# Optimization experiments

Hardware: AMD Instinct MI355X
Metric: run time of the kernel (lower is better)

Reference implementation:

```python
import jax, jax.numpy as jnp
import numpy as np

N = 20000      # nodes
E = 640000     # edges
F = 128        # input features
H = 256        # hidden dim
G = 64         # graphs in batch


def setup_inputs() -> dict:
    key = jax.random.key(0)
    ks = jax.random.split(key, 24)
    w = lambda k, sh: (jax.random.normal(k, sh, jnp.float32) * 0.05)
    inp = {
        'x': jax.random.normal(ks[0], (N, F), jnp.float32),
        'edge_index': jax.random.randint(ks[1], (2, E), 0, N, dtype=jnp.int32),
        'batch': jnp.sort(jax.random.randint(ks[2], (N,), 0, G, dtype=jnp.int32)),
        # GCN stack
        'gcn_w1': w(ks[3], (F, H)), 'gcn_b1': jnp.zeros((H,), jnp.float32),
        'gcn_w2': w(ks[4], (H, H)), 'gcn_b2': jnp.zeros((H,), jnp.float32),
        'gcn_w3': w(ks[5], (H, H)), 'gcn_b3': jnp.zeros((H,), jnp.float32),
        'gcn_w4': w(ks[6], (H, H)), 'gcn_b4': jnp.zeros((H,), jnp.float32),
        # EdgeConv 1: Linear(2F,H) -> ReLU -> Linear(H,H)
        'ec1_w1': w(ks[7], (2 * F, H)), 'ec1_b1': jnp.zeros((H,), jnp.float32),
        'ec1_w2': w(ks[8], (H, H)),     'ec1_b2': jnp.zeros((H,), jnp.float32),
        # EdgeConv 2: Linear(2H,H) -> ReLU -> Linear(H,H)
        'ec2_w1': w(ks[9], (2 * H, H)), 'ec2_b1': jnp.zeros((H,), jnp.float32),
        'ec2_w2': w(ks[10], (H, H)),    'ec2_b2': jnp.zeros((H,), jnp.float32),
        # head
        'fc1_w': w(ks[11], (2 * H, H)), 'fc1_b': jnp.zeros((H,), jnp.float32),
        'out_w': w(ks[12], (H, 1)),     'out_b': jnp.zeros((1,), jnp.float32),
    }
    return inp


def _gcn_conv(x, W, b, src, dst, n):
    # PyG GCNConv: add self loops, symmetric deg^-1/2 normalization, scatter-sum.
    h = x @ W                                        # [n, H]
    loops = jnp.arange(n, dtype=src.dtype)
    s = jnp.concatenate([src, loops])
    d = jnp.concatenate([dst, loops])
    deg = jax.ops.segment_sum(jnp.ones(s.shape[0], x.dtype), d, num_segments=n)
    dinv = jnp.where(deg > 0, jax.lax.rsqrt(deg), 0.0)
    norm = (dinv[s] * dinv[d])[:, None]              # [E+n, 1]
    return jax.ops.segment_sum(h[s] * norm, d, num_segments=n) + b


def _edge_conv(x, w1, b1, w2, b2, src, dst, n):
    # PyG EdgeConv: msg = MLP([x_i, x_j - x_i]), max-aggregate at target i.
    xi = x[dst]
    xj = x[src]
    m = jnp.concatenate([xi, xj - xi], axis=1)       # [E, 2*d]
    m = jax.nn.relu(m @ w1 + b1) @ w2 + b2           # [E, H]
    out = jax.ops.segment_max(m, dst, num_segments=n)
    return jnp.where(jnp.isfinite(out), out, 0.0)    # empty segments -> 0


def reference(x, edge_index, batch,
              gcn_w1, gcn_b1, gcn_w2, gcn_b2, gcn_w3, gcn_b3, gcn_w4, gcn_b4,
              ec1_w1, ec1_b1, ec1_w2, ec1_b2, ec2_w1, ec2_b1, ec2_w2, ec2_b2,
              fc1_w, fc1_b, out_w, out_b):
    n = x.shape[0]
    src, dst = edge_index[0], edge_index[1]
    relu = jax.nn.relu
    # GCN branch (dropout is identity at inference)
    xg = relu(_gcn_conv(x, gcn_w1, gcn_b1, src, dst, n))
    xg = relu(_gcn_conv(xg, gcn_w2, gcn_b2, src, dst, n))
    xg = relu(_gcn_conv(xg, gcn_w3, gcn_b3, src, dst, n))
    xg = relu(_gcn_conv(xg, gcn_w4, gcn_b4, src, dst, n))
    # EdgeConv branch
    xe = relu(_edge_conv(x, ec1_w1, ec1_b1, ec1_w2, ec1_b2, src, dst, n))
    xe = relu(_edge_conv(xe, ec2_w1, ec2_b1, ec2_w2, ec2_b2, src, dst, n))
    # pool per graph + head
    x_cat = jnp.concatenate([xg, xe], axis=1)        # [n, 512]
    g = jax.ops.segment_sum(x_cat, batch, num_segments=G)  # [G, 512]
    g = relu(g @ fc1_w + fc1_b)
    return g @ out_w + out_b                          # [G, 1]
```

## Files before the change

### kernel.cpp

```cpp
#include <hip/hip_runtime.h>

#define HD 256

typedef __attribute__((ext_vector_type(8))) __bf16 bf16x8;
typedef __attribute__((ext_vector_type(4))) float f32x4;

static __device__ __forceinline__ float relu_f(float x){ return x > 0.f ? x : 0.f; }

static __device__ __forceinline__ void split_cvt(const float* m8, bf16x8& vh, bf16x8& vl){
    #pragma unroll
    for (int j = 0; j < 8; j++){
        float m = m8[j];
        __bf16 h = (__bf16)m;
        vh[j] = h;
        vl[j] = (__bf16)(m - (float)h);
    }
}

__global__ void k_count(const int* __restrict__ dst, int* __restrict__ cnt, int E){
    int i = blockIdx.x * blockDim.x + threadIdx.x;
    if (i < E) atomicAdd(&cnt[dst[i]], 1);
}

__global__ void k_dinv(const int* __restrict__ cnt, float* __restrict__ dinv, int n){
    int i = blockIdx.x * blockDim.x + threadIdx.x;
    if (i < n) dinv[i] = 1.0f / sqrtf((float)(cnt[i] + 1));
}

__global__ void k_scan(const int* __restrict__ cnt, int* __restrict__ row_ptr, int n){
    __shared__ int lds[1024];
    int t = threadIdx.x;
    int carry = 0;
    for (int base = 0; base < n; base += 1024){
        int idx = base + t;
        int v = (idx < n) ? cnt[idx] : 0;
        __syncthreads();
        lds[t] = v;
        __syncthreads();
        for (int off = 1; off < 1024; off <<= 1){
            int add = (t >= off) ? lds[t - off] : 0;
            __syncthreads();
            lds[t] += add;
            __syncthreads();
        }
        int incl = lds[t];
        if (idx < n) row_ptr[idx] = carry + incl - v;
        carry += lds[1023];
    }
    if (t == 0) row_ptr[n] = carry;
}

__global__ void k_fill(const int* __restrict__ src, const int* __restrict__ dst,
                       const int* __restrict__ row_ptr, int* __restrict__ fill,
                       int* __restrict__ csr_src, int* __restrict__ csr_dst, int E){
    int i = blockIdx.x * blockDim.x + threadIdx.x;
    if (i < E){
        int d = dst[i];
        int pos = row_ptr[d] + atomicAdd(&fill[d], 1);
        csr_src[pos] = src[i];
        csr_dst[pos] = d;
    }
}

__global__ void k_wpack(const float* __restrict__ W, __bf16* __restrict__ ph,
                        __bf16* __restrict__ pl, int K){
    int total = (K >> 5) * 8192;
    int idx = blockIdx.x * blockDim.x + threadIdx.x;
    if (idx >= total) return;
    int j = idx & 7, g = (idx >> 3) & 3, c = (idx >> 5) & 255, ks = idx >> 13;
    int k = ks * 32 + g * 8 + j;
    float v = W[(size_t)k * HD + c];
    __bf16 h = (__bf16)v;
    ph[idx] = h;
    pl[idx] = (__bf16)(v - (float)h);
}

__global__ void k_wdiff(const float* __restrict__ w, float* __restrict__ wd, int K){
    int i = blockIdx.x * blockDim.x + threadIdx.x;
    if (i < K * HD) wd[i] = w[i] - w[K * HD + i];
}

__global__ __launch_bounds__(256) void k_gemm_mfma(
    const float* __restrict__ A,
    const __bf16* __restrict__ Wph, const __bf16* __restrict__ Wpl,
    const float* __restrict__ bias,
    float* __restrict__ C, int M, int K)
{
    __shared__ __bf16 mh[2][64][40];
    __shared__ __bf16 ml[2][64][40];
    int t = threadIdx.x;
    int m0 = blockIdx.x * 64;
    const int w = t >> 6, fr = t & 15, fg = (t & 63) >> 4;
    const int srow = t >> 2, skb = (t & 3) * 8;
    int ar = m0 + srow; if (ar >= M) ar = M - 1;
    const float* Arow = A + (size_t)ar * K + skb;
    const int c0 = w * 64 + fr;
    const int KS = K >> 5;

    f32x4 acc[4][4];
    #pragma unroll
    for (int i = 0; i < 4; i++)
        #pragma unroll
        for (int j = 0; j < 4; j++) acc[i][j] = (f32x4){0.f, 0.f, 0.f, 0.f};

    {
        float4 a0 = *(const float4*)(Arow);
        float4 a1 = *(const float4*)(Arow + 4);
        float m8[8] = {a0.x, a0.y, a0.z, a0.w, a1.x, a1.y, a1.z, a1.w};
        bf16x8 vh, vl;
        split_cvt(m8, vh, vl);
        *(bf16x8*)&mh[0][srow][skb] = vh;
        *(bf16x8*)&ml[0][srow][skb] = vl;
    }

    for (int ks = 0; ks < KS; ++ks){
        float4 a0, a1;
        if (ks + 1 < KS){
            a0 = *(const float4*)(Arow + (ks + 1) * 32);
            a1 = *(const float4*)(Arow + (ks + 1) * 32 + 4);
        }
        bf16x8 bh[4], bl[4];
        #pragma unroll
        for (int nf = 0; nf < 4; nf++){
            size_t bi = ((size_t)(ks * 256 + c0 + nf * 16) * 4 + fg) * 8;
            bh[nf] = *(const bf16x8*)(Wph + bi);
            bl[nf] = *(const bf16x8*)(Wpl + bi);
        }
        __syncthreads();
        const int cb = ks & 1;
        #pragma unroll
        for (int mf = 0; mf < 4; mf++){
            bf16x8 ah = *(const bf16x8*)&mh[cb][mf * 16 + fr][fg * 8];
            bf16x8 al = *(const bf16x8*)&ml[cb][mf * 16 + fr][fg * 8];
            #pragma unroll
            for (int nf = 0; nf < 4; nf++){
                acc[mf][nf] = __builtin_amdgcn_mfma_f32_16x16x32_bf16(ah, bh[nf], acc[mf][nf], 0, 0, 0);
                acc[mf][nf] = __builtin_amdgcn_mfma_f32_16x16x32_bf16(al, bh[nf], acc[mf][nf], 0, 0, 0);
                acc[mf][nf] = __builtin_amdgcn_mfma_f32_16x16x32_bf16(ah, bl[nf], acc[mf][nf], 0, 0, 0);
            }
        }
        if (ks + 1 < KS){
            float m8[8] = {a0.x, a0.y, a0.z, a0.w, a1.x, a1.y, a1.z, a1.w};
            bf16x8 vh, vl;
            split_cvt(m8, vh, vl);
            *(bf16x8*)&mh[cb ^ 1][srow][skb] = vh;
            *(bf16x8*)&ml[cb ^ 1][srow][skb] = vl;
        }
    }

    float bj[4];
    #pragma unroll
    for (int nf = 0; nf < 4; nf++) bj[nf] = bias ? bias[c0 + nf * 16] : 0.f;
    #pragma unroll
    for (int mf = 0; mf < 4; mf++)
        #pragma unroll
        for (int reg = 0; reg < 4; reg++){
            int row = m0 + mf * 16 + fg * 4 + reg;
            if (row < M){
                #pragma unroll
                for (int nf = 0; nf < 4; nf++)
                    C[(size_t)row * HD + c0 + nf * 16] = acc[mf][nf][reg] + bj[nf];
            }
        }
}

__global__ __launch_bounds__(256) void k_gcn_agg(const float* __restrict__ h,
                                                 const float* __restrict__ dinv,
                                                 const int* __restrict__ row_ptr,
                                                 const int* __restrict__ csr_src,
                                                 const float* __restrict__ bias,
                                                 float* __restrict__ out, int n){
    int wid = threadIdx.x >> 6, lane = threadIdx.x & 63;
    int i = blockIdx.x * 4 + wid;
    if (i >= n) return;
    float di = dinv[i];
    const float4* hp = (const float4*)h;
    float4 v = hp[(size_t)i * 64 + lane];
    float ax = v.x * di, ay = v.y * di, az = v.z * di, aw = v.w * di;
    int e0 = row_ptr[i], e1 = row_ptr[i + 1];
    for (int e = e0; e < e1; e++){
        int s = csr_src[e];
        float ds = dinv[s];
        float4 u = hp[(size_t)s * 64 + lane];
        ax += u.x * ds; ay += u.y * ds; az += u.z * ds; aw += u.w * ds;
    }
    const float4 b = ((const float4*)bias)[lane];
    float4 o;
    o.x = relu_f(ax * di + b.x);
    o.y = relu_f(ay * di + b.y);
    o.z = relu_f(az * di + b.z);
    o.w = relu_f(aw * di + b.w);
    ((float4*)out)[(size_t)i * 64 + lane] = o;
}

__global__ __launch_bounds__(256) void k_edge_mfma(
    const float* __restrict__ A, const float* __restrict__ B,
    const __bf16* __restrict__ Wph, const __bf16* __restrict__ Wpl,
    const float* __restrict__ bias,
    const int* __restrict__ csr_src, const int* __restrict__ csr_dst,
    float* __restrict__ out, int E)
{
    __shared__ __bf16 mh[2][64][40];
    __shared__ __bf16 ml[2][64][40];
    __shared__ int sdst[64], ssrc[64];
    int t = threadIdx.x;
    int p0 = blockIdx.x * 64;
    if (t < 64){
        int e = p0 + t; if (e >= E) e = E - 1;
        sdst[t] = csr_dst[e];
        ssrc[t] = csr_src[e];
    }
    __syncthreads();

    const int w  = t >> 6;
    const int fr = t & 15;
    const int fg = (t & 63) >> 4;
    const int srow = t >> 2, skb = (t & 3) * 8;
    const float* Arow = A + (size_t)sdst[srow] * HD + skb;
    const float* Brow = B + (size_t)ssrc[srow] * HD + skb;
    const int c0 = w * 64 + fr;

    f32x4 acc[4][4];
    #pragma unroll
    for (int i = 0; i < 4; i++)
        #pragma unroll
        for (int j = 0; j < 4; j++) acc[i][j] = (f32x4){0.f, 0.f, 0.f, 0.f};

    {
        float4 a0 = *(const float4*)(Arow);
        float4 a1 = *(const float4*)(Arow + 4);
        float4 g0 = *(const float4*)(Brow);
        float4 g1 = *(const float4*)(Brow + 4);
        float m8[8] = {relu_f(a0.x + g0.x), relu_f(a0.y + g0.y), relu_f(a0.z + g0.z), relu_f(a0.w + g0.w),
                       relu_f(a1.x + g1.x), relu_f(a1.y + g1.y), relu_f(a1.z + g1.z), relu_f(a1.w + g1.w)};
        bf16x8 vh, vl;
        split_cvt(m8, vh, vl);
        *(bf16x8*)&mh[0][srow][skb] = vh;
        *(bf16x8*)&ml[0][srow][skb] = vl;
    }

    for (int ks = 0; ks < 8; ++ks){
        float4 a0, a1, g0, g1;
        if (ks < 7){
            a0 = *(const float4*)(Arow + (ks + 1) * 32);
            a1 = *(const float4*)(Arow + (ks + 1) * 32 + 4);
            g0 = *(const float4*)(Brow + (ks + 1) * 32);
            g1 = *(const float4*)(Brow + (ks + 1) * 32 + 4);
        }
        bf16x8 bh[4], bl[4];
        #pragma unroll
        for (int nf = 0; nf < 4; nf++){
            size_t bi = ((size_t)(ks * 256 + c0 + nf * 16) * 4 + fg) * 8;
            bh[nf] = *(const bf16x8*)(Wph + bi);
            bl[nf] = *(const bf16x8*)(Wpl + bi);
        }
        __syncthreads();
        const int cb = ks & 1;
        #pragma unroll
        for (int mf = 0; mf < 4; mf++){
            bf16x8 ah = *(const bf16x8*)&mh[cb][mf * 16 + fr][fg * 8];
            bf16x8 al = *(const bf16x8*)&ml[cb][mf * 16 + fr][fg * 8];
            #pragma unroll
            for (int nf = 0; nf < 4; nf++){
                acc[mf][nf] = __builtin_amdgcn_mfma_f32_16x16x32_bf16(ah, bh[nf], acc[mf][nf], 0, 0, 0);
                acc[mf][nf] = __builtin_amdgcn_mfma_f32_16x16x32_bf16(al, bh[nf], acc[mf][nf], 0, 0, 0);
                acc[mf][nf] = __builtin_amdgcn_mfma_f32_16x16x32_bf16(ah, bl[nf], acc[mf][nf], 0, 0, 0);
            }
        }
        if (ks < 7){
            float m8[8] = {relu_f(a0.x + g0.x), relu_f(a0.y + g0.y), relu_f(a0.z + g0.z), relu_f(a0.w + g0.w),
                           relu_f(a1.x + g1.x), relu_f(a1.y + g1.y), relu_f(a1.z + g1.z), relu_f(a1.w + g1.w)};
            bf16x8 vh, vl;
            split_cvt(m8, vh, vl);
            *(bf16x8*)&mh[cb ^ 1][srow][skb] = vh;
            *(bf16x8*)&ml[cb ^ 1][srow][skb] = vl;
        }
    }

    float bj[4];
    #pragma unroll
    for (int nf = 0; nf < 4; nf++) bj[nf] = bias[c0 + nf * 16];
    int curd = sdst[fg * 4];
    float v[4];
    #pragma unroll
    for (int nf = 0; nf < 4; nf++) v[nf] = acc[0][nf][0] + bj[nf];
    #pragma unroll
    for (int mf = 0; mf < 4; mf++){
        #pragma unroll
        for (int reg = 0; reg < 4; reg++){
            if (mf == 0 && reg == 0) continue;
            int d = sdst[mf * 16 + fg * 4 + reg];
            if (d != curd){
                #pragma unroll
                for (int nf = 0; nf < 4; nf++)
                    if (v[nf] > 0.f)
                        atomicMax((int*)(out + (size_t)curd * HD + c0 + nf * 16), __float_as_int(v[nf]));
                curd = d;
                #pragma unroll
                for (int nf = 0; nf < 4; nf++) v[nf] = acc[mf][nf][reg] + bj[nf];
            } else {
                #pragma unroll
                for (int nf = 0; nf < 4; nf++) v[nf] = fmaxf(v[nf], acc[mf][nf][reg] + bj[nf]);
            }
        }
    }
    #pragma unroll
    for (int nf = 0; nf < 4; nf++)
        if (v[nf] > 0.f)
            atomicMax((int*)(out + (size_t)curd * HD + c0 + nf * 16), __float_as_int(v[nf]));
}

__global__ __launch_bounds__(512) void k_pool(const float* __restrict__ xg,
                                              const float* __restrict__ xe,
                                              const int* __restrict__ batch,
                                              float* __restrict__ gpool, int n){
    int g = blockIdx.x, t = threadIdx.x;
    int lo, hi;
    { int l = 0, h = n; while (l < h){ int m = (l + h) >> 1; if (batch[m] < g) l = m + 1; else h = m; } lo = l; }
    { int l = lo, h = n; while (l < h){ int m = (l + h) >> 1; if (batch[m] < g + 1) l = m + 1; else h = m; } hi = l; }
    const float* sp = (t < 256) ? (xg + t) : (xe + (t - 256));
    float a0 = 0.f, a1 = 0.f;
    int i = lo;
    for (; i + 1 < hi; i += 2){
        a0 += sp[(size_t)i * HD];
        a1 += sp[(size_t)(i + 1) * HD];
    }
    if (i < hi) a0 += sp[(size_t)i * HD];
    gpool[g * 512 + t] = a0 + a1;
}

__global__ __launch_bounds__(256) void k_head(const float* __restrict__ gpool,
                                              const float* __restrict__ w1,
                                              const float* __restrict__ b1,
                                              const float* __restrict__ w2,
                                              const float* __restrict__ b2,
                                              float* __restrict__ out){
    __shared__ float red[256];
    int g = blockIdx.x, t = threadIdx.x;
    float acc = b1[t];
    const float* gp = gpool + g * 512;
    #pragma unroll 4
    for (int k = 0; k < 512; k++) acc += gp[k] * w1[k * HD + t];
    red[t] = relu_f(acc) * w2[t];
    __syncthreads();
    for (int s = 128; s > 0; s >>= 1){
        if (t < s) red[t] += red[t + s];
        __syncthreads();
    }
    if (t == 0) out[g] = red[0] + b2[0];
}

extern "C" void kernel_launch(void* const* d_in, const int* in_sizes, int n_in,
                              void* d_out, int out_size, void* d_ws, size_t ws_size,
                              hipStream_t stream){
    const float* x      = (const float*)d_in[0];
    const int*   ei     = (const int*)d_in[1];
    const int*   batch  = (const int*)d_in[2];
    const float* gcn_w[4] = {(const float*)d_in[3], (const float*)d_in[5], (const float*)d_in[7], (const float*)d_in[9]};
    const float* gcn_b[4] = {(const float*)d_in[4], (const float*)d_in[6], (const float*)d_in[8], (const float*)d_in[10]};
    const float* ec1_w1 = (const float*)d_in[11]; const float* ec1_b1 = (const float*)d_in[12];
    const float* ec1_w2 = (const float*)d_in[13]; const float* ec1_b2 = (const float*)d_in[14];
    const float* ec2_w1 = (const float*)d_in[15]; const float* ec2_b1 = (const float*)d_in[16];
    const float* ec2_w2 = (const float*)d_in[17]; const float* ec2_b2 = (const float*)d_in[18];
    const float* fc1_w  = (const float*)d_in[19]; const float* fc1_b  = (const float*)d_in[20];
    const float* out_w  = (const float*)d_in[21]; const float* out_b  = (const float*)d_in[22];

    const int N = in_sizes[2];
    const int E = in_sizes[1] / 2;
    const int F = in_sizes[0] / N;
    const int* src = ei;
    const int* dst = ei + E;
    const int GB64 = (N + 63) / 64;

    char* w = (char*)d_ws;
    auto alloc = [&](size_t bytes) -> char* {
        char* p = w;
        w += (bytes + 255) & ~(size_t)255;
        return p;
    };
    int*   cnt     = (int*)alloc((size_t)N * 4);
    int*   fillc   = (int*)alloc((size_t)N * 4);
    int*   row_ptr = (int*)alloc((size_t)(N + 1) * 4);
    int*   csr_src = (int*)alloc((size_t)E * 4);
    int*   csr_dst = (int*)alloc((size_t)E * 4);
    float* dinv    = (float*)alloc((size_t)N * 4);
    float* wd      = (float*)alloc((size_t)HD * HD * 4);
    float* act     = (float*)alloc((size_t)N * HD * 4);
    float* hbuf    = (float*)alloc((size_t)N * HD * 4);
    float* Bbuf    = (float*)alloc((size_t)N * HD * 4);
    float* xebuf   = (float*)alloc((size_t)N * HD * 4);
    float* gpool   = (float*)alloc((size_t)64 * 512 * 4);
    auto packa = [&](int K) -> __bf16* { return (__bf16*)alloc((size_t)(K / 32) * 8192 * 2); };
    __bf16* pg1h = packa(128); __bf16* pg1l = packa(128);
    __bf16* pg2h = packa(256); __bf16* pg2l = packa(256);
    __bf16* pg3h = packa(256); __bf16* pg3l = packa(256);
    __bf16* pg4h = packa(256); __bf16* pg4l = packa(256);
    __bf16* pe1ah = packa(128); __bf16* pe1al = packa(128);
    __bf16* pe1bh = packa(128); __bf16* pe1bl = packa(128);
    __bf16* pe2ah = packa(256); __bf16* pe2al = packa(256);
    __bf16* pe2bh = packa(256); __bf16* pe2bl = packa(256);
    __bf16* w2h1 = packa(256); __bf16* w2l1 = packa(256);
    __bf16* w2h2 = packa(256); __bf16* w2l2 = packa(256);

    auto wpack = [&](const float* W, __bf16* ph, __bf16* pl, int K){
        int total = (K / 32) * 8192;
        k_wpack<<<(total + 255) / 256, 256, 0, stream>>>(W, ph, pl, K);
    };

    hipMemsetAsync(cnt, 0, (size_t)N * 4, stream);
    hipMemsetAsync(fillc, 0, (size_t)N * 4, stream);
    k_count<<<(E + 255) / 256, 256, 0, stream>>>(dst, cnt, E);
    k_dinv<<<(N + 255) / 256, 256, 0, stream>>>(cnt, dinv, N);
    k_scan<<<1, 1024, 0, stream>>>(cnt, row_ptr, N);
    k_fill<<<(E + 255) / 256, 256, 0, stream>>>(src, dst, row_ptr, fillc, csr_src, csr_dst, E);

    wpack(gcn_w[0], pg1h, pg1l, F);
    wpack(gcn_w[1], pg2h, pg2l, HD);
    wpack(gcn_w[2], pg3h, pg3l, HD);
    wpack(gcn_w[3], pg4h, pg4l, HD);
    k_wdiff<<<(F * HD + 255) / 256, 256, 0, stream>>>(ec1_w1, wd, F);
    wpack(wd, pe1ah, pe1al, F);
    wpack(ec1_w1 + (size_t)F * HD, pe1bh, pe1bl, F);
    k_wdiff<<<(HD * HD + 255) / 256, 256, 0, stream>>>(ec2_w1, wd, HD);
    wpack(wd, pe2ah, pe2al, HD);
    wpack(ec2_w1 + (size_t)HD * HD, pe2bh, pe2bl, HD);
    wpack(ec1_w2, w2h1, w2l1, HD);
    wpack(ec2_w2, w2h2, w2l2, HD);

    k_gemm_mfma<<<GB64, 256, 0, stream>>>(x, pg1h, pg1l, nullptr, hbuf, N, F);
    k_gcn_agg<<<N / 4, 256, 0, stream>>>(hbuf, dinv, row_ptr, csr_src, gcn_b[0], act, N);
    const __bf16* pgh[3] = {pg2h, pg3h, pg4h};
    const __bf16* pgl[3] = {pg2l, pg3l, pg4l};
    for (int l = 0; l < 3; l++){
        k_gemm_mfma<<<GB64, 256, 0, stream>>>(act, pgh[l], pgl[l], nullptr, hbuf, N, HD);
        k_gcn_agg<<<N / 4, 256, 0, stream>>>(hbuf, dinv, row_ptr, csr_src, gcn_b[l + 1], act, N);
    }

    k_gemm_mfma<<<GB64, 256, 0, stream>>>(x, pe1ah, pe1al, ec1_b1, hbuf, N, F);
    k_gemm_mfma<<<GB64, 256, 0, stream>>>(x, pe1bh, pe1bl, nullptr, Bbuf, N, F);
    hipMemsetAsync(xebuf, 0, (size_t)N * HD * 4, stream);
    k_edge_mfma<<<E / 64, 256, 0, stream>>>(hbuf, Bbuf, w2h1, w2l1, ec1_b2, csr_src, csr_dst, xebuf, E);

    k_gemm_mfma<<<GB64, 256, 0, stream>>>(xebuf, pe2ah, pe2al, ec2_b1, hbuf, N, HD);
    k_gemm_mfma<<<GB64, 256, 0, stream>>>(xebuf, pe2bh, pe2bl, nullptr, Bbuf, N, HD);
    hipMemsetAsync(xebuf, 0, (size_t)N * HD * 4, stream);
    k_edge_mfma<<<E / 64, 256, 0, stream>>>(hbuf, Bbuf, w2h2, w2l2, ec2_b2, csr_src, csr_dst, xebuf, E);

    k_pool<<<64, 512, 0, stream>>>(act, xebuf, batch, gpool, N);
    k_head<<<64, 256, 0, stream>>>(gpool, fc1_w, fc1_b, out_w, out_b, (float*)d_out);
}
```

Measured before the change: 1.445 ms.

## Use 512-thread GEMM blocks, remap edge blocks per XCD, batch weight packing

New measurement: 1.332 ms. 7.8% less time.

```diff
diff --git a/kernel.cpp b/kernel.cpp
--- a/kernel.cpp
+++ b/kernel.cpp
@@ -3,17 +3,18 @@
 #define HD 256
 
 typedef __attribute__((ext_vector_type(8))) __bf16 bf16x8;
+typedef __attribute__((ext_vector_type(4))) __bf16 bf16x4;
 typedef __attribute__((ext_vector_type(4))) float f32x4;
 
 static __device__ __forceinline__ float relu_f(float x){ return x > 0.f ? x : 0.f; }
 
-static __device__ __forceinline__ void split_cvt(const float* m8, bf16x8& vh, bf16x8& vl){
-    #pragma unroll
-    for (int j = 0; j < 8; j++){
-        float m = m8[j];
-        __bf16 h = (__bf16)m;
+static __device__ __forceinline__ void split4(const float* m, bf16x4& vh, bf16x4& vl){
+    #pragma unroll
+    for (int j = 0; j < 4; j++){
+        float v = m[j];
+        __bf16 h = (__bf16)v;
         vh[j] = h;
-        vl[j] = (__bf16)(m - (float)h);
+        vl[j] = (__bf16)(v - (float)h);
     }
 }
 
@@ -62,25 +63,24 @@
     }
 }
 
-__global__ void k_wpack(const float* __restrict__ W, __bf16* __restrict__ ph,
-                        __bf16* __restrict__ pl, int K){
-    int total = (K >> 5) * 8192;
-    int idx = blockIdx.x * blockDim.x + threadIdx.x;
+struct PackDesc { const float* src; const float* src2; __bf16* ph; __bf16* pl; int K; int pad; };
+struct PackArgs { PackDesc d[10]; };
+
+__global__ void k_wpack_all(PackArgs a){
+    PackDesc p = a.d[blockIdx.y];
+    int total = (p.K >> 5) * 8192;
+    int idx = blockIdx.x * 256 + threadIdx.x;
     if (idx >= total) return;
     int j = idx & 7, g = (idx >> 3) & 3, c = (idx >> 5) & 255, ks = idx >> 13;
     int k = ks * 32 + g * 8 + j;
-    float v = W[(size_t)k * HD + c];
+    float v = p.src[(size_t)k * HD + c];
+    if (p.src2) v -= p.src2[(size_t)k * HD + c];
     __bf16 h = (__bf16)v;
-    ph[idx] = h;
-    pl[idx] = (__bf16)(v - (float)h);
-}
-
-__global__ void k_wdiff(const float* __restrict__ w, float* __restrict__ wd, int K){
-    int i = blockIdx.x * blockDim.x + threadIdx.x;
-    if (i < K * HD) wd[i] = w[i] - w[K * HD + i];
-}
-
-__global__ __launch_bounds__(256) void k_gemm_mfma(
+    p.ph[idx] = h;
+    p.pl[idx] = (__bf16)(v - (float)h);
+}
+
+__global__ __launch_bounds__(512, 4) void k_gemm_mfma(
     const float* __restrict__ A,
     const __bf16* __restrict__ Wph, const __bf16* __restrict__ Wpl,
     const float* __restrict__ bias,
@@ -91,37 +91,33 @@
     int t = threadIdx.x;
     int m0 = blockIdx.x * 64;
     const int w = t >> 6, fr = t & 15, fg = (t & 63) >> 4;
-    const int srow = t >> 2, skb = (t & 3) * 8;
+    const int srow = t >> 3, skb = (t & 7) * 4;
     int ar = m0 + srow; if (ar >= M) ar = M - 1;
     const float* Arow = A + (size_t)ar * K + skb;
-    const int c0 = w * 64 + fr;
+    const int c0 = w * 32 + fr;
     const int KS = K >> 5;
 
-    f32x4 acc[4][4];
+    f32x4 acc[4][2];
     #pragma unroll
     for (int i = 0; i < 4; i++)
         #pragma unroll
-        for (int j = 0; j < 4; j++) acc[i][j] = (f32x4){0.f, 0.f, 0.f, 0.f};
+        for (int j = 0; j < 2; j++) acc[i][j] = (f32x4){0.f, 0.f, 0.f, 0.f};
 
     {
-        float4 a0 = *(const float4*)(Arow);
-        float4 a1 = *(const float4*)(Arow + 4);
-        float m8[8] = {a0.x, a0.y, a0.z, a0.w, a1.x, a1.y, a1.z, a1.w};
-        bf16x8 vh, vl;
-        split_cvt(m8, vh, vl);
-        *(bf16x8*)&mh[0][srow][skb] = vh;
-        *(bf16x8*)&ml[0][srow][skb] = vl;
+        float4 av = *(const float4*)(Arow);
+        float m4[4] = {av.x, av.y, av.z, av.w};
+        bf16x4 vh, vl;
+        split4(m4, vh, vl);
+        *(bf16x4*)&mh[0][srow][skb] = vh;
+        *(bf16x4*)&ml[0][srow][skb] = vl;
     }
 
     for (int ks = 0; ks < KS; ++ks){
-        float4 a0, a1;
-        if (ks + 1 < KS){
-            a0 = *(const float4*)(Arow + (ks + 1) * 32);
-            a1 = *(const float4*)(Arow + (ks + 1) * 32 + 4);
-        }
-        bf16x8 bh[4], bl[4];
-        #pragma unroll
-        for (int nf = 0; nf < 4; nf++){
+        float4 av;
+        if (ks + 1 < KS) av = *(const float4*)(Arow + (ks + 1) * 32);
+        bf16x8 bh[2], bl[2];
+        #pragma unroll
+        for (int nf = 0; nf < 2; nf++){
             size_t bi = ((size_t)(ks * 256 + c0 + nf * 16) * 4 + fg) * 8;
             bh[nf] = *(const bf16x8*)(Wph + bi);
             bl[nf] = *(const bf16x8*)(Wpl + bi);
@@ -133,24 +129,24 @@
             bf16x8 ah = *(const bf16x8*)&mh[cb][mf * 16 + fr][fg * 8];
             bf16x8 al = *(const bf16x8*)&ml[cb][mf * 16 + fr][fg * 8];
             #pragma unroll
-            for (int nf = 0; nf < 4; nf++){
+            for (int nf = 0; nf < 2; nf++){
                 acc[mf][nf] = __builtin_amdgcn_mfma_f32_16x16x32_bf16(ah, bh[nf], acc[mf][nf], 0, 0, 0);
                 acc[mf][nf] = __builtin_amdgcn_mfma_f32_16x16x32_bf16(al, bh[nf], acc[mf][nf], 0, 0, 0);
                 acc[mf][nf] = __builtin_amdgcn_mfma_f32_16x16x32_bf16(ah, bl[nf], acc[mf][nf], 0, 0, 0);
             }
         }
         if (ks + 1 < KS){
-            float m8[8] = {a0.x, a0.y, a0.z, a0.w, a1.x, a1.y, a1.z, a1.w};
-            bf16x8 vh, vl;
-            split_cvt(m8, vh, vl);
-            *(bf16x8*)&mh[cb ^ 1][srow][skb] = vh;
-            *(bf16x8*)&ml[cb ^ 1][srow][skb] = vl;
-        }
-    }
-
-    float bj[4];
-    #pragma unroll
-    for (int nf = 0; nf < 4; nf++) bj[nf] = bias ? bias[c0 + nf * 16] : 0.f;
+            float m4[4] = {av.x, av.y, av.z, av.w};
+            bf16x4 vh, vl;
+            split4(m4, vh, vl);
+            *(bf16x4*)&mh[cb ^ 1][srow][skb] = vh;
+            *(bf16x4*)&ml[cb ^ 1][srow][skb] = vl;
+        }
+    }
+
+    float bj[2];
+    #pragma unroll
+    for (int nf = 0; nf < 2; nf++) bj[nf] = bias ? bias[c0 + nf * 16] : 0.f;
     #pragma unroll
     for (int mf = 0; mf < 4; mf++)
         #pragma unroll
@@ -158,7 +154,7 @@
             int row = m0 + mf * 16 + fg * 4 + reg;
             if (row < M){
                 #pragma unroll
-                for (int nf = 0; nf < 4; nf++)
+                for (int nf = 0; nf < 2; nf++)
                     C[(size_t)row * HD + c0 + nf * 16] = acc[mf][nf][reg] + bj[nf];
             }
         }
@@ -193,7 +189,7 @@
     ((float4*)out)[(size_t)i * 64 + lane] = o;
 }
 
-__global__ __launch_bounds__(256) void k_edge_mfma(
+__global__ __launch_bounds__(512, 4) void k_edge_mfma(
     const float* __restrict__ A, const float* __restrict__ B,
     const __bf16* __restrict__ Wph, const __bf16* __restrict__ Wpl,
     const float* __restrict__ bias,
@@ -204,7 +200,11 @@
     __shared__ __bf16 ml[2][64][40];
     __shared__ int sdst[64], ssrc[64];
     int t = threadIdx.x;
-    int p0 = blockIdx.x * 64;
+    int nwg = gridDim.x;
+    int q = nwg >> 3, r = nwg & 7;
+    int xc = blockIdx.x & 7;
+    int bid = (xc < r ? xc * (q + 1) : r * (q + 1) + (xc - r) * q) + (blockIdx.x >> 3);
+    int p0 = bid * 64;
     if (t < 64){
         int e = p0 + t; if (e >= E) e = E - 1;
         sdst[t] = csr_dst[e];
@@ -215,41 +215,36 @@
     const int w  = t >> 6;
     const int fr = t & 15;
     const int fg = (t & 63) >> 4;
-    const int srow = t >> 2, skb = (t & 3) * 8;
+    const int srow = t >> 3, skb = (t & 7) * 4;
     const float* Arow = A + (size_t)sdst[srow] * HD + skb;
     const float* Brow = B + (size_t)ssrc[srow] * HD + skb;
-    const int c0 = w * 64 + fr;
-
-    f32x4 acc[4][4];
+    const int c0 = w * 32 + fr;
+
+    f32x4 acc[4][2];
     #pragma unroll
     for (int i = 0; i < 4; i++)
         #pragma unroll
-        for (int j = 0; j < 4; j++) acc[i][j] = (f32x4){0.f, 0.f, 0.f, 0.f};
+        for (int j = 0; j < 2; j++) acc[i][j] = (f32x4){0.f, 0.f, 0.f, 0.f};
 
     {
-        float4 a0 = *(const float4*)(Arow);
-        float4 a1 = *(const float4*)(Arow + 4);
-        float4 g0 = *(const float4*)(Brow);
-        float4 g1 = *(const float4*)(Brow + 4);
-        float m8[8] = {relu_f(a0.x + g0.x), relu_f(a0.y + g0.y), relu_f(a0.z + g0.z), relu_f(a0.w + g0.w),
-                       relu_f(a1.x + g1.x), relu_f(a1.y + g1.y), relu_f(a1.z + g1.z), relu_f(a1.w + g1.w)};
-        bf16x8 vh, vl;
-        split_cvt(m8, vh, vl);
-        *(bf16x8*)&mh[0][srow][skb] = vh;
-        *(bf16x8*)&ml[0][srow][skb] = vl;
+        float4 a = *(const float4*)(Arow);
+        float4 g = *(const float4*)(Brow);
+        float m4[4] = {relu_f(a.x + g.x), relu_f(a.y + g.y), relu_f(a.z + g.z), relu_f(a.w + g.w)};
+        bf16x4 vh, vl;
+        split4(m4, vh, vl);
+        *(bf16x4*)&mh[0][srow][skb] = vh;
+        *(bf16x4*)&ml[0][srow][skb] = vl;
     }
 
     for (int ks = 0; ks < 8; ++ks){
-        float4 a0, a1, g0, g1;
+        float4 a, g;
         if (ks < 7){
-            a0 = *(const float4*)(Arow + (ks + 1) * 32);
-            a1 = *(const float4*)(Arow + (ks + 1) * 32 + 4);
-            g0 = *(const float4*)(Brow + (ks + 1) * 32);
-            g1 = *(const float4*)(Brow + (ks + 1) * 32 + 4);
-        }
-        bf16x8 bh[4], bl[4];
-        #pragma unroll
-        for (int nf = 0; nf < 4; nf++){
+            a = *(const float4*)(Arow + (ks + 1) * 32);
+            g = *(const float4*)(Brow + (ks + 1) * 32);
+        }
+        bf16x8 bh[2], bl[2];
+        #pragma unroll
+        for (int nf = 0; nf < 2; nf++){
             size_t bi = ((size_t)(ks * 256 + c0 + nf * 16) * 4 + fg) * 8;
             bh[nf] = *(const bf16x8*)(Wph + bi);
             bl[nf] = *(const bf16x8*)(Wpl + bi);
@@ -261,29 +256,28 @@
             bf16x8 ah = *(const bf16x8*)&mh[cb][mf * 16 + fr][fg * 8];
             bf16x8 al = *(const bf16x8*)&ml[cb][mf * 16 + fr][fg * 8];
             #pragma unroll
-            for (int nf = 0; nf < 4; nf++){
+            for (int nf = 0; nf < 2; nf++){
                 acc[mf][nf] = __builtin_amdgcn_mfma_f32_16x16x32_bf16(ah, bh[nf], acc[mf][nf], 0, 0, 0);
                 acc[mf][nf] = __builtin_amdgcn_mfma_f32_16x16x32_bf16(al, bh[nf], acc[mf][nf], 0, 0, 0);
                 acc[mf][nf] = __builtin_amdgcn_mfma_f32_16x16x32_bf16(ah, bl[nf], acc[mf][nf], 0, 0, 0);
             }
         }
         if (ks < 7){
-            float m8[8] = {relu_f(a0.x + g0.x), relu_f(a0.y + g0.y), relu_f(a0.z + g0.z), relu_f(a0.w + g0.w),
-                           relu_f(a1.x + g1.x), relu_f(a1.y + g1.y), relu_f(a1.z + g1.z), relu_f(a1.w + g1.w)};
-            bf16x8 vh, vl;
-            split_cvt(m8, vh, vl);
-            *(bf16x8*)&mh[cb ^ 1][srow][skb] = vh;
-            *(bf16x8*)&ml[cb ^ 1][srow][skb] = vl;
-        }
-    }
-
-    float bj[4];
-    #pragma unroll
-    for (int nf = 0; nf < 4; nf++) bj[nf] = bias[c0 + nf * 16];
+            float m4[4] = {relu_f(a.x + g.x), relu_f(a.y + g.y), relu_f(a.z + g.z), relu_f(a.w + g.w)};
+            bf16x4 vh, vl;
+            split4(m4, vh, vl);
+            *(bf16x4*)&mh[cb ^ 1][srow][skb] = vh;
+            *(bf16x4*)&ml[cb ^ 1][srow][skb] = vl;
+        }
+    }
+
+    float bj[2];
+    #pragma unroll
+    for (int nf = 0; nf < 2; nf++) bj[nf] = bias[c0 + nf * 16];
     int curd = sdst[fg * 4];
-    float v[4];
-    #pragma unroll
-    for (int nf = 0; nf < 4; nf++) v[nf] = acc[0][nf][0] + bj[nf];
+    float v[2];
+    #pragma unroll
+    for (int nf = 0; nf < 2; nf++) v[nf] = acc[0][nf][0] + bj[nf];
     #pragma unroll
     for (int mf = 0; mf < 4; mf++){
         #pragma unroll
@@ -292,20 +286,20 @@
             int d = sdst[mf * 16 + fg * 4 + reg];
             if (d != curd){
                 #pragma unroll
-                for (int nf = 0; nf < 4; nf++)
+                for (int nf = 0; nf < 2; nf++)
                     if (v[nf] > 0.f)
                         atomicMax((int*)(out + (size_t)curd * HD + c0 + nf * 16), __float_as_int(v[nf]));
                 curd = d;
                 #pragma unroll
-                for (int nf = 0; nf < 4; nf++) v[nf] = acc[mf][nf][reg] + bj[nf];
+                for (int nf = 0; nf < 2; nf++) v[nf] = acc[mf][nf][reg] + bj[nf];
             } else {
                 #pragma unroll
-                for (int nf = 0; nf < 4; nf++) v[nf] = fmaxf(v[nf], acc[mf][nf][reg] + bj[nf]);
+                for (int nf = 0; nf < 2; nf++) v[nf] = fmaxf(v[nf], acc[mf][nf][reg] + bj[nf]);
             }
         }
     }
     #pragma unroll
-    for (int nf = 0; nf < 4; nf++)
+    for (int nf = 0; nf < 2; nf++)
         if (v[nf] > 0.f)
             atomicMax((int*)(out + (size_t)curd * HD + c0 + nf * 16), __float_as_int(v[nf]));
 }
@@ -371,6 +365,7 @@
     const int* src = ei;
     const int* dst = ei + E;
     const int GB64 = (N + 63) / 64;
+    const int EB   = (E + 63) / 64;
 
     char* w = (char*)d_ws;
     auto alloc = [&](size_t bytes) -> char* {
@@ -384,13 +379,12 @@
     int*   csr_src = (int*)alloc((size_t)E * 4);
     int*   csr_dst = (int*)alloc((size_t)E * 4);
     float* dinv    = (float*)alloc((size_t)N * 4);
-    float* wd      = (float*)alloc((size_t)HD * HD * 4);
     float* act     = (float*)alloc((size_t)N * HD * 4);
     float* hbuf    = (float*)alloc((size_t)N * HD * 4);
     float* Bbuf    = (float*)alloc((size_t)N * HD * 4);
     float* xebuf   = (float*)alloc((size_t)N * HD * 4);
     float* gpool   = (float*)alloc((size_t)64 * 512 * 4);
-    auto packa = [&](int K) -> __bf16* { return (__bf16*)alloc((size_t)(K / 32) * 8192 * 2); };
+    auto packa = [&](int K) -> __bf16* { return (__bf16*)alloc((size_t)K * 256 * 2); };
     __bf16* pg1h = packa(128); __bf16* pg1l = packa(128);
     __bf16* pg2h = packa(256); __bf16* pg2l = packa(256);
     __bf16* pg3h = packa(256); __bf16* pg3l = packa(256);
@@ -402,11 +396,6 @@
     __bf16* w2h1 = packa(256); __bf16* w2l1 = packa(256);
     __bf16* w2h2 = packa(256); __bf16* w2l2 = packa(256);
 
-    auto wpack = [&](const float* W, __bf16* ph, __bf16* pl, int K){
-        int total = (K / 32) * 8192;
-        k_wpack<<<(total + 255) / 256, 256, 0, stream>>>(W, ph, pl, K);
-    };
-
     hipMemsetAsync(cnt, 0, (size_t)N * 4, stream);
     hipMemsetAsync(fillc, 0, (size_t)N * 4, stream);
     k_count<<<(E + 255) / 256, 256, 0, stream>>>(dst, cnt, E);
@@ -414,37 +403,37 @@
     k_scan<<<1, 1024, 0, stream>>>(cnt, row_ptr, N);
     k_fill<<<(E + 255) / 256, 256, 0, stream>>>(src, dst, row_ptr, fillc, csr_src, csr_dst, E);
 
-    wpack(gcn_w[0], pg1h, pg1l, F);
-    wpack(gcn_w[1], pg2h, pg2l, HD);
-    wpack(gcn_w[2], pg3h, pg3l, HD);
-    wpack(gcn_w[3], pg4h, pg4l, HD);
-    k_wdiff<<<(F * HD + 255) / 256, 256, 0, stream>>>(ec1_w1, wd, F);
-    wpack(wd, pe1ah, pe1al, F);
-    wpack(ec1_w1 + (size_t)F * HD, pe1bh, pe1bl, F);
-    k_wdiff<<<(HD * HD + 255) / 256, 256, 0, stream>>>(ec2_w1, wd, HD);
-    wpack(wd, pe2ah, pe2al, HD);
-    wpack(ec2_w1 + (size_t)HD * HD, pe2bh, pe2bl, HD);
-    wpack(ec1_w2, w2h1, w2l1, HD);
-    wpack(ec2_w2, w2h2, w2l2, HD);
-
-    k_gemm_mfma<<<GB64, 256, 0, stream>>>(x, pg1h, pg1l, nullptr, hbuf, N, F);
-    k_gcn_agg<<<N / 4, 256, 0, stream>>>(hbuf, dinv, row_ptr, csr_src, gcn_b[0], act, N);
+    PackArgs pa;
+    pa.d[0] = {gcn_w[0],                  nullptr,                    pg1h,  pg1l,  F,  0};
+    pa.d[1] = {gcn_w[1],                  nullptr,                    pg2h,  pg2l,  HD, 0};
+    pa.d[2] = {gcn_w[2],                  nullptr,                    pg3h,  pg3l,  HD, 0};
+    pa.d[3] = {gcn_w[3],                  nullptr,                    pg4h,  pg4l,  HD, 0};
+    pa.d[4] = {ec1_w1,                    ec1_w1 + (size_t)F * HD,    pe1ah, pe1al, F,  0};
+    pa.d[5] = {ec1_w1 + (size_t)F * HD,   nullptr,                    pe1bh, pe1bl, F,  0};
+    pa.d[6] = {ec2_w1,                    ec2_w1 + (size_t)HD * HD,   pe2ah, pe2al, HD, 0};
+    pa.d[7] = {ec2_w1 + (size_t)HD * HD,  nullptr,                    pe2bh, pe2bl, HD, 0};
+    pa.d[8] = {ec1_w2,                    nullptr,                    w2h1,  w2l1,  HD, 0};
+    pa.d[9] = {ec2_w2,                    nullptr,                    w2h2,  w2l2,  HD, 0};
+    k_wpack_all<<<dim3(256, 10), 256, 0, stream>>>(pa);
+
+    k_gemm_mfma<<<GB64, 512, 0, stream>>>(x, pg1h, pg1l, nullptr, hbuf, N, F);
+    k_gcn_agg<<<(N + 3) / 4, 256, 0, stream>>>(hbuf, dinv, row_ptr, csr_src, gcn_b[0], act, N);
     const __bf16* pgh[3] = {pg2h, pg3h, pg4h};
     const __bf16* pgl[3] = {pg2l, pg3l, pg4l};
     for (int l = 0; l < 3; l++){
-        k_gemm_mfma<<<GB64, 256, 0, stream>>>(act, pgh[l], pgl[l], nullptr, hbuf, N, HD);
-        k_gcn_agg<<<N / 4, 256, 0, stream>>>(hbuf, dinv, row_ptr, csr_src, gcn_b[l + 1], act, N);
-    }
-
-    k_gemm_mfma<<<GB64, 256, 0, stream>>>(x, pe1ah, pe1al, ec1_b1, hbuf, N, F);
-    k_gemm_mfma<<<GB64, 256, 0, stream>>>(x, pe1bh, pe1bl, nullptr, Bbuf, N, F);
+        k_gemm_mfma<<<GB64, 512, 0, stream>>>(act, pgh[l], pgl[l], nullptr, hbuf, N, HD);
+        k_gcn_agg<<<(N + 3) / 4, 256, 0, stream>>>(hbuf, dinv, row_ptr, csr_src, gcn_b[l + 1], act, N);
+    }
+
+    k_gemm_mfma<<<GB64, 512, 0, stream>>>(x, pe1ah, pe1al, ec1_b1, hbuf, N, F);
+    k_gemm_mfma<<<GB64, 512, 0, stream>>>(x, pe1bh, pe1bl, nullptr, Bbuf, N, F);
     hipMemsetAsync(xebuf, 0, (size_t)N * HD * 4, stream);
-    k_edge_mfma<<<E / 64, 256, 0, stream>>>(hbuf, Bbuf, w2h1, w2l1, ec1_b2, csr_src, csr_dst, xebuf, E);
-
-    k_gemm_mfma<<<GB64, 256, 0, stream>>>(xebuf, pe2ah, pe2al, ec2_b1, hbuf, N, HD);
-    k_gemm_mfma<<<GB64, 256, 0, stream>>>(xebuf, pe2bh, pe2bl, nullptr, Bbuf, N, HD);
+    k_edge_mfma<<<EB, 512, 0, stream>>>(hbuf, Bbuf, w2h1, w2l1, ec1_b2, csr_src, csr_dst, xebuf, E);
+
+    k_gemm_mfma<<<GB64, 512, 0, stream>>>(xebuf, pe2ah, pe2al, ec2_b1, hbuf, N, HD);
+    k_gemm_mfma<<<GB64, 512, 0, stream>>>(xebuf, pe2bh, pe2bl, nullptr, Bbuf, N, HD);
     hipMemsetAsync(xebuf, 0, (size_t)N * HD * 4, stream);
-    k_edge_mfma<<<E / 64, 256, 0, stream>>>(hbuf, Bbuf, w2h2, w2l2, ec2_b2, csr_src, csr_dst, xebuf, E);
+    k_edge_mfma<<<EB, 512, 0, stream>>>(hbuf, Bbuf, w2h2, w2l2, ec2_b2, csr_src, csr_dst, xebuf, E);
 
     k_pool<<<64, 512, 0, stream>>>(act, xebuf, batch, gpool, N);
     k_head<<<64, 256, 0, stream>>>(gpool, fc1_w, fc1_b, out_w, out_b, (float*)d_out);
```
